# Performance work log

Measured on AMD Instinct MI355X. Metric: run time of the kernel, lower is better.

## Reference

```python
import jax, jax.numpy as jnp
import numpy as np

N = 4096
PED_SPEED = 1.34   # desired pedestrian speed (m/s)
K = 2.0            # goal-attraction gain
ALPHA = 10.66      # repulsion strength
PED_RADIUS = 0.3
PED_MASS = 60.0
BETTA = 0.71       # repulsion range
DT = 0.4
COST_A = 1.0       # goal-progress weight
COST_B = 1.0       # blame (proximity) weight
COST_E = 1.0       # blame length scale
EPS = 1e-8


def calc_forces(state, goals):
    pos = state[:, 0:2]            # [N,2]
    vel = state[:, 2:4]            # [N,2]
    # O(N^2) pairwise social repulsion
    delta = pos[:, None, :] - pos[None, :, :]                    # [N,N,2]
    dist = jnp.sqrt(jnp.sum(delta * delta, axis=-1) + EPS)       # [N,N]
    mag = ALPHA * jnp.exp((2.0 * PED_RADIUS - dist) / BETTA)     # [N,N]
    mag = mag * (1.0 - jnp.eye(pos.shape[0], dtype=pos.dtype))   # zero self-force
    rep_force = jnp.sum((mag / dist)[..., None] * delta, axis=1)  # [N,2]
    # attraction toward goal: relax velocity to desired velocity
    to_goal = goals - pos
    gd = jnp.sqrt(jnp.sum(to_goal * to_goal, axis=-1, keepdims=True) + EPS)
    attr_force = K * PED_MASS * (PED_SPEED * to_goal / gd - vel)
    return rep_force, attr_force


def pose_propagation(F, state):
    pos = state[:, 0:2]
    vel = state[:, 2:4]
    vel_new = vel + (F / PED_MASS) * DT
    speed = jnp.sqrt(jnp.sum(vel_new * vel_new, axis=-1, keepdims=True) + EPS)
    vel_new = vel_new * jnp.minimum(1.0, PED_SPEED / speed)  # clamp to max speed
    pos_new = pos + vel_new * DT
    return jnp.concatenate([pos_new, vel_new], axis=1)      # [N,4]


def calc_cost_function(goals, robot_init_pose, state, observed_state):
    pos = state[:, 0:2]
    robot_pose = pos[0]  # agent 0 is the robot
    goal_vec = goals[0] - robot_init_pose
    pg = jnp.dot(pos[0] - robot_init_pose, goal_vec) / (jnp.sqrt(jnp.sum(goal_vec * goal_vec)) + EPS)
    dist_rp = jnp.sqrt(jnp.sum((pos - robot_pose) ** 2, axis=-1) + EPS)  # [N]
    blame = COST_B * jnp.exp(-dist_rp / COST_E)
    dev = jnp.sum((pos - observed_state[:, 0:2]) ** 2, axis=-1)
    return -COST_A * pg + blame + dev  # [N]


def setup_inputs():
    key = jax.random.key(0)
    k1, k2, k3, k4 = jax.random.split(key, 4)
    scale = jnp.array([10.0, 10.0, 1.0, 1.0], dtype=jnp.float32)
    state = jax.random.normal(k1, (N, 4), dtype=jnp.float32) * scale
    goals = jax.random.normal(k2, (N, 2), dtype=jnp.float32) * 10.0
    robot_init_pose = jax.random.normal(k3, (2,), dtype=jnp.float32) * 10.0
    observed_state = jax.random.normal(k4, (N, 4), dtype=jnp.float32) * scale
    cost = jnp.zeros((N, 1), dtype=jnp.float32)
    return {"state": state, "cost": cost, "goals": goals,
            "robot_init_pose": robot_init_pose, "observed_state": observed_state}


def reference(state, cost, goals, robot_init_pose, observed_state):
    rf, af = calc_forces(state, goals)
    F = rf + af
    out = pose_propagation(F, state)
    temp = calc_cost_function(goals, robot_init_pose, out, observed_state)
    cost_new = cost + temp.reshape(-1, 1)
    return out, cost_new
```

## Files before the change

kernel.cpp:

```cpp
#include <hip/hip_runtime.h>

#define N 4096
#define NBJ 64
#define EPS 1e-8f

typedef float v2f __attribute__((ext_vector_type(2)));

__global__ __launch_bounds__(256) void rep_pairs(const float4* __restrict__ state4,
                                                 float2* __restrict__ part) {
    __shared__ float sx[64];
    __shared__ float sy[64];
    const int tid = threadIdx.x;
    const int jb  = blockIdx.y;
    const int i   = blockIdx.x * 256 + tid;

    if (tid < 64) {
        const float4 s = state4[jb * 64 + tid];
        sx[tid] = s.x;
        sy[tid] = s.y;
    }
    const float4 si = state4[i];
    __syncthreads();

    const float C1 = 1.44269504088896340736f / 0.71f;
    const float C0 = 0.6f * C1 + 3.41414351f;

    const v2f xi  = {si.x, si.x};
    const v2f yi  = {si.y, si.y};
    const v2f eps = {EPS, EPS};
    v2f fx0 = {0.f, 0.f}, fy0 = {0.f, 0.f};
    v2f fx1 = {0.f, 0.f}, fy1 = {0.f, 0.f};

#pragma unroll 8
    for (int jj = 0; jj < 64; jj += 4) {
        {
            const v2f X = *(const v2f*)&sx[jj];
            const v2f Y = *(const v2f*)&sy[jj];
            const v2f dx = xi - X;
            const v2f dy = yi - Y;
            const v2f r2 = dx * dx + (dy * dy + eps);
            v2f inv; inv.x = __builtin_amdgcn_rsqf(r2.x);
                     inv.y = __builtin_amdgcn_rsqf(r2.y);
            const v2f d   = r2 * inv;
            const v2f arg = C0 - C1 * d;
            v2f e; e.x = __builtin_amdgcn_exp2f(arg.x);
                   e.y = __builtin_amdgcn_exp2f(arg.y);
            const v2f coef = e * inv;
            fx0 += coef * dx;
            fy0 += coef * dy;
        }
        {
            const v2f X = *(const v2f*)&sx[jj + 2];
            const v2f Y = *(const v2f*)&sy[jj + 2];
            const v2f dx = xi - X;
            const v2f dy = yi - Y;
            const v2f r2 = dx * dx + (dy * dy + eps);
            v2f inv; inv.x = __builtin_amdgcn_rsqf(r2.x);
                     inv.y = __builtin_amdgcn_rsqf(r2.y);
            const v2f d   = r2 * inv;
            const v2f arg = C0 - C1 * d;
            v2f e; e.x = __builtin_amdgcn_exp2f(arg.x);
                   e.y = __builtin_amdgcn_exp2f(arg.y);
            const v2f coef = e * inv;
            fx1 += coef * dx;
            fy1 += coef * dy;
        }
    }
    const v2f fxs = fx0 + fx1, fys = fy0 + fy1;
    part[(size_t)jb * N + i] = make_float2(fxs.x + fxs.y, fys.x + fys.y);
}

__global__ __launch_bounds__(256) void finalize(const float4* __restrict__ state4,
                                                const float*  __restrict__ cost_in,
                                                const float*  __restrict__ goals,
                                                const float*  __restrict__ rip,
                                                const float4* __restrict__ obs4,
                                                const float2* __restrict__ part,
                                                float*        __restrict__ out) {
    __shared__ float4 red[4][64];
    __shared__ float2 s_p0;
    const int tid = threadIdx.x;
    const int ip  = tid & 63;
    const int ks  = tid >> 6;
    const int i0  = blockIdx.x * 128 + ip * 2;
    const float4* p4 = (const float4*)part;

    float4 acc = make_float4(0.f, 0.f, 0.f, 0.f);
    for (int k = ks * 16; k < ks * 16 + 16; ++k) {
        const float4 p = p4[(size_t)k * (N / 2) + (i0 >> 1)];
        acc.x += p.x; acc.y += p.y; acc.z += p.z; acc.w += p.w;
    }
    red[ks][ip] = acc;

    if (tid < 64) {
        float2 f0 = part[(size_t)tid * N];
#pragma unroll
        for (int off = 32; off > 0; off >>= 1) {
            f0.x += __shfl_down(f0.x, off);
            f0.y += __shfl_down(f0.y, off);
        }
        if (tid == 0) {
            const float4 s0 = state4[0];
            const float gx = goals[0] - s0.x, gy = goals[1] - s0.y;
            const float gd = sqrtf(fmaf(gx, gx, fmaf(gy, gy, EPS)));
            const float Fx0 = f0.x + 120.f * (1.34f * gx / gd - s0.z);
            const float Fy0 = f0.y + 120.f * (1.34f * gy / gd - s0.w);
            float vnx = fmaf(Fx0, 0.4f / 60.f, s0.z);
            float vny = fmaf(Fy0, 0.4f / 60.f, s0.w);
            const float sp  = sqrtf(fmaf(vnx, vnx, fmaf(vny, vny, EPS)));
            const float fac = fminf(1.f, 1.34f / sp);
            vnx *= fac; vny *= fac;
            s_p0 = make_float2(fmaf(vnx, 0.4f, s0.x), fmaf(vny, 0.4f, s0.y));
        }
    }
    __syncthreads();

    if (ks == 0) {
        float4 a = red[0][ip];
        const float4 b = red[1][ip], c = red[2][ip], d4 = red[3][ip];
        a.x += b.x + c.x + d4.x;
        a.y += b.y + c.y + d4.y;
        a.z += b.z + c.z + d4.z;
        a.w += b.w + c.w + d4.w;

        const float4 g2 = ((const float4*)goals)[i0 >> 1];
        const float2 ci = ((const float2*)cost_in)[i0 >> 1];
        const float rx = rip[0], ry = rip[1];
        const float gvx = goals[0] - rx, gvy = goals[1] - ry;
        const float inv_gl = 1.f / (sqrtf(gvx * gvx + gvy * gvy) + EPS);
        const float p0x = s_p0.x, p0y = s_p0.y;
        const float pg = ((p0x - rx) * gvx + (p0y - ry) * gvy) * inv_gl;

        float2 cost_out;
#pragma unroll
        for (int u = 0; u < 2; ++u) {
            const int ia = i0 + u;
            float Fx = u ? a.z : a.x;
            float Fy = u ? a.w : a.y;
            const float4 s = state4[ia];
            const float gx = (u ? g2.z : g2.x) - s.x;
            const float gy = (u ? g2.w : g2.y) - s.y;
            const float gd = sqrtf(fmaf(gx, gx, fmaf(gy, gy, EPS)));
            Fx += 120.f * (1.34f * gx / gd - s.z);
            Fy += 120.f * (1.34f * gy / gd - s.w);
            float vnx = fmaf(Fx, 0.4f / 60.f, s.z);
            float vny = fmaf(Fy, 0.4f / 60.f, s.w);
            const float sp  = sqrtf(fmaf(vnx, vnx, fmaf(vny, vny, EPS)));
            const float fac = fminf(1.f, 1.34f / sp);
            vnx *= fac; vny *= fac;
            const float pnx = fmaf(vnx, 0.4f, s.x);
            const float pny = fmaf(vny, 0.4f, s.y);

            ((float4*)out)[ia] = make_float4(pnx, pny, vnx, vny);

            const float ddx = pnx - p0x, ddy = pny - p0y;
            const float dist_rp = sqrtf(fmaf(ddx, ddx, fmaf(ddy, ddy, EPS)));
            const float blame = __expf(-dist_rp);
            const float4 ob = obs4[ia];
            const float dev = (pnx - ob.x) * (pnx - ob.x) + (pny - ob.y) * (pny - ob.y);
            const float cv = (u ? ci.y : ci.x) + (-pg + blame + dev);
            if (u) cost_out.y = cv; else cost_out.x = cv;
        }
        ((float2*)(out + 4 * N))[i0 >> 1] = cost_out;
    }
}

extern "C" void kernel_launch(void* const* d_in, const int* in_sizes, int n_in,
                              void* d_out, int out_size, void* d_ws, size_t ws_size,
                              hipStream_t stream) {
    const float* state = (const float*)d_in[0];
    const float* cost  = (const float*)d_in[1];
    const float* goals = (const float*)d_in[2];
    const float* rip   = (const float*)d_in[3];
    const float* obs   = (const float*)d_in[4];
    float* out   = (float*)d_out;
    float2* part = (float2*)d_ws;

    rep_pairs<<<dim3(16, NBJ), 256, 0, stream>>>((const float4*)state, part);
    finalize<<<N / 128, 256, 0, stream>>>((const float4*)state, cost, goals, rip,
                                          (const float4*)obs, part, out);
}
```

Measured before the change: 69.52 us.

## Fuse pairwise repulsion and finalize into one kernel with in-block reduction

After: 69.26 us. About the same (-0.4%).

```diff
diff --git a/kernel.cpp b/kernel.cpp
--- a/kernel.cpp
+++ b/kernel.cpp
@@ -1,167 +1,177 @@
 #include <hip/hip_runtime.h>
 
 #define N 4096
-#define NBJ 64
 #define EPS 1e-8f
+#define BLK 512
+#define APB 8
 
 typedef float v2f __attribute__((ext_vector_type(2)));
 
-__global__ __launch_bounds__(256) void rep_pairs(const float4* __restrict__ state4,
-                                                 float2* __restrict__ part) {
-    __shared__ float sx[64];
-    __shared__ float sy[64];
+__global__ __launch_bounds__(BLK) void fused(const float4* __restrict__ state4,
+                                             const float*  __restrict__ cost_in,
+                                             const float*  __restrict__ goals,
+                                             const float*  __restrict__ rip,
+                                             const float4* __restrict__ obs4,
+                                             float*        __restrict__ out) {
+    __shared__ float  sx[N];
+    __shared__ float  sy[N];
+    __shared__ float4 red[BLK / 64][4];
+    __shared__ float2 red0[BLK / 64];
+
     const int tid = threadIdx.x;
-    const int jb  = blockIdx.y;
-    const int i   = blockIdx.x * 256 + tid;
+    const int blk = blockIdx.x;
 
-    if (tid < 64) {
-        const float4 s = state4[jb * 64 + tid];
-        sx[tid] = s.x;
-        sy[tid] = s.y;
+#pragma unroll
+    for (int m = 0; m < 4; ++m) {
+        const int j0 = 2 * tid + 1024 * m;
+        const float4 a = state4[j0];
+        const float4 b = state4[j0 + 1];
+        *(v2f*)&sx[j0] = (v2f){a.x, b.x};
+        *(v2f*)&sy[j0] = (v2f){a.y, b.y};
     }
-    const float4 si = state4[i];
+
+    const int il = tid & 3;
+    const int ks = tid >> 2;
+    const int a0 = blk * APB + 2 * il;
+    const float4 sA = state4[a0];
+    const float4 sB = state4[a0 + 1];
     __syncthreads();
 
     const float C1 = 1.44269504088896340736f / 0.71f;
     const float C0 = 0.6f * C1 + 3.41414351f;
 
-    const v2f xi  = {si.x, si.x};
-    const v2f yi  = {si.y, si.y};
-    const v2f eps = {EPS, EPS};
-    v2f fx0 = {0.f, 0.f}, fy0 = {0.f, 0.f};
-    v2f fx1 = {0.f, 0.f}, fy1 = {0.f, 0.f};
+    const v2f eps2 = {EPS, EPS};
+    const v2f xA = {sA.x, sA.x}, yA = {sA.y, sA.y};
+    const v2f xB = {sB.x, sB.x}, yB = {sB.y, sB.y};
+    v2f fxA = {0.f, 0.f}, fyA = {0.f, 0.f};
+    v2f fxB = {0.f, 0.f}, fyB = {0.f, 0.f};
 
-#pragma unroll 8
-    for (int jj = 0; jj < 64; jj += 4) {
-        {
-            const v2f X = *(const v2f*)&sx[jj];
-            const v2f Y = *(const v2f*)&sy[jj];
-            const v2f dx = xi - X;
-            const v2f dy = yi - Y;
-            const v2f r2 = dx * dx + (dy * dy + eps);
-            v2f inv; inv.x = __builtin_amdgcn_rsqf(r2.x);
-                     inv.y = __builtin_amdgcn_rsqf(r2.y);
-            const v2f d   = r2 * inv;
-            const v2f arg = C0 - C1 * d;
-            v2f e; e.x = __builtin_amdgcn_exp2f(arg.x);
-                   e.y = __builtin_amdgcn_exp2f(arg.y);
-            const v2f coef = e * inv;
-            fx0 += coef * dx;
-            fy0 += coef * dy;
-        }
-        {
-            const v2f X = *(const v2f*)&sx[jj + 2];
-            const v2f Y = *(const v2f*)&sy[jj + 2];
-            const v2f dx = xi - X;
-            const v2f dy = yi - Y;
-            const v2f r2 = dx * dx + (dy * dy + eps);
-            v2f inv; inv.x = __builtin_amdgcn_rsqf(r2.x);
-                     inv.y = __builtin_amdgcn_rsqf(r2.y);
-            const v2f d   = r2 * inv;
-            const v2f arg = C0 - C1 * d;
-            v2f e; e.x = __builtin_amdgcn_exp2f(arg.x);
-                   e.y = __builtin_amdgcn_exp2f(arg.y);
-            const v2f coef = e * inv;
-            fx1 += coef * dx;
-            fy1 += coef * dy;
+#pragma unroll
+    for (int c = 0; c < 8; ++c) {
+        const int j0 = (ks << 5) + (((c + ks) & 7) << 2);
+        const float4 X = *(const float4*)&sx[j0];
+        const float4 Y = *(const float4*)&sy[j0];
+        const v2f Xp[2] = {{X.x, X.y}, {X.z, X.w}};
+        const v2f Yp[2] = {{Y.x, Y.y}, {Y.z, Y.w}};
+#pragma unroll
+        for (int h = 0; h < 2; ++h) {
+            {
+                const v2f dx = xA - Xp[h];
+                const v2f dy = yA - Yp[h];
+                const v2f r2 = dx * dx + (dy * dy + eps2);
+                v2f inv; inv.x = __builtin_amdgcn_rsqf(r2.x);
+                         inv.y = __builtin_amdgcn_rsqf(r2.y);
+                const v2f d   = r2 * inv;
+                const v2f arg = C0 - C1 * d;
+                v2f e; e.x = __builtin_amdgcn_exp2f(arg.x);
+                       e.y = __builtin_amdgcn_exp2f(arg.y);
+                const v2f coef = e * inv;
+                fxA += coef * dx;
+                fyA += coef * dy;
+            }
+            {
+                const v2f dx = xB - Xp[h];
+                const v2f dy = yB - Yp[h];
+                const v2f r2 = dx * dx + (dy * dy + eps2);
+                v2f inv; inv.x = __builtin_amdgcn_rsqf(r2.x);
+                         inv.y = __builtin_amdgcn_rsqf(r2.y);
+                const v2f d   = r2 * inv;
+                const v2f arg = C0 - C1 * d;
+                v2f e; e.x = __builtin_amdgcn_exp2f(arg.x);
+                       e.y = __builtin_amdgcn_exp2f(arg.y);
+                const v2f coef = e * inv;
+                fxB += coef * dx;
+                fyB += coef * dy;
+            }
         }
     }
-    const v2f fxs = fx0 + fx1, fys = fy0 + fy1;
-    part[(size_t)jb * N + i] = make_float2(fxs.x + fxs.y, fys.x + fys.y);
-}
 
-__global__ __launch_bounds__(256) void finalize(const float4* __restrict__ state4,
-                                                const float*  __restrict__ cost_in,
-                                                const float*  __restrict__ goals,
-                                                const float*  __restrict__ rip,
-                                                const float4* __restrict__ obs4,
-                                                const float2* __restrict__ part,
-                                                float*        __restrict__ out) {
-    __shared__ float4 red[4][64];
-    __shared__ float2 s_p0;
-    const int tid = threadIdx.x;
-    const int ip  = tid & 63;
-    const int ks  = tid >> 6;
-    const int i0  = blockIdx.x * 128 + ip * 2;
-    const float4* p4 = (const float4*)part;
-
-    float4 acc = make_float4(0.f, 0.f, 0.f, 0.f);
-    for (int k = ks * 16; k < ks * 16 + 16; ++k) {
-        const float4 p = p4[(size_t)k * (N / 2) + (i0 >> 1)];
-        acc.x += p.x; acc.y += p.y; acc.z += p.z; acc.w += p.w;
-    }
-    red[ks][ip] = acc;
-
-    if (tid < 64) {
-        float2 f0 = part[(size_t)tid * N];
+    float f0x = 0.f, f0y = 0.f;
+    {
+        const float x0 = sx[0], y0 = sy[0];
 #pragma unroll
-        for (int off = 32; off > 0; off >>= 1) {
-            f0.x += __shfl_down(f0.x, off);
-            f0.y += __shfl_down(f0.y, off);
-        }
-        if (tid == 0) {
-            const float4 s0 = state4[0];
-            const float gx = goals[0] - s0.x, gy = goals[1] - s0.y;
-            const float gd = sqrtf(fmaf(gx, gx, fmaf(gy, gy, EPS)));
-            const float Fx0 = f0.x + 120.f * (1.34f * gx / gd - s0.z);
-            const float Fy0 = f0.y + 120.f * (1.34f * gy / gd - s0.w);
-            float vnx = fmaf(Fx0, 0.4f / 60.f, s0.z);
-            float vny = fmaf(Fy0, 0.4f / 60.f, s0.w);
-            const float sp  = sqrtf(fmaf(vnx, vnx, fmaf(vny, vny, EPS)));
-            const float fac = fminf(1.f, 1.34f / sp);
-            vnx *= fac; vny *= fac;
-            s_p0 = make_float2(fmaf(vnx, 0.4f, s0.x), fmaf(vny, 0.4f, s0.y));
+        for (int m = 0; m < 8; ++m) {
+            const int j = tid + (m << 9);
+            const float dx = x0 - sx[j];
+            const float dy = y0 - sy[j];
+            const float r2 = fmaf(dx, dx, fmaf(dy, dy, EPS));
+            const float inv = __builtin_amdgcn_rsqf(r2);
+            const float d   = r2 * inv;
+            const float coef = __builtin_amdgcn_exp2f(fmaf(-C1, d, C0)) * inv;
+            f0x = fmaf(coef, dx, f0x);
+            f0y = fmaf(coef, dy, f0y);
         }
     }
+
+    float FxA = fxA.x + fxA.y, FyA = fyA.x + fyA.y;
+    float FxB = fxB.x + fxB.y, FyB = fyB.x + fyB.y;
+#pragma unroll
+    for (int off = 4; off <= 32; off <<= 1) {
+        FxA += __shfl_xor(FxA, off);
+        FyA += __shfl_xor(FyA, off);
+        FxB += __shfl_xor(FxB, off);
+        FyB += __shfl_xor(FyB, off);
+    }
+#pragma unroll
+    for (int off = 1; off <= 32; off <<= 1) {
+        f0x += __shfl_xor(f0x, off);
+        f0y += __shfl_xor(f0y, off);
+    }
+    const int wv = tid >> 6, ln = tid & 63;
+    if (ln < 4)  red[wv][ln] = make_float4(FxA, FyA, FxB, FyB);
+    if (ln == 0) red0[wv] = make_float2(f0x, f0y);
     __syncthreads();
 
-    if (ks == 0) {
-        float4 a = red[0][ip];
-        const float4 b = red[1][ip], c = red[2][ip], d4 = red[3][ip];
-        a.x += b.x + c.x + d4.x;
-        a.y += b.y + c.y + d4.y;
-        a.z += b.z + c.z + d4.z;
-        a.w += b.w + c.w + d4.w;
+    if (tid < APB) {
+        float Fx = 0.f, Fy = 0.f, F0x = 0.f, F0y = 0.f;
+#pragma unroll
+        for (int w = 0; w < BLK / 64; ++w) {
+            const float4 r = red[w][tid >> 1];
+            Fx += (tid & 1) ? r.z : r.x;
+            Fy += (tid & 1) ? r.w : r.y;
+            const float2 r0 = red0[w];
+            F0x += r0.x; F0y += r0.y;
+        }
 
-        const float4 g2 = ((const float4*)goals)[i0 >> 1];
-        const float2 ci = ((const float2*)cost_in)[i0 >> 1];
+        const float4 s0 = state4[0];
+        const float g0x = goals[0] - s0.x, g0y = goals[1] - s0.y;
+        const float gd0 = sqrtf(fmaf(g0x, g0x, fmaf(g0y, g0y, EPS)));
+        F0x += 120.f * (1.34f * g0x / gd0 - s0.z);
+        F0y += 120.f * (1.34f * g0y / gd0 - s0.w);
+        float v0x = fmaf(F0x, 0.4f / 60.f, s0.z);
+        float v0y = fmaf(F0y, 0.4f / 60.f, s0.w);
+        const float sp0 = sqrtf(fmaf(v0x, v0x, fmaf(v0y, v0y, EPS)));
+        const float fc0 = fminf(1.f, 1.34f / sp0);
+        v0x *= fc0; v0y *= fc0;
+        const float p0x = fmaf(v0x, 0.4f, s0.x);
+        const float p0y = fmaf(v0y, 0.4f, s0.y);
+
+        const int ia = blk * APB + tid;
+        const float4 s = state4[ia];
+        const float gx = goals[2 * ia]     - s.x;
+        const float gy = goals[2 * ia + 1] - s.y;
+        const float gd = sqrtf(fmaf(gx, gx, fmaf(gy, gy, EPS)));
+        Fx += 120.f * (1.34f * gx / gd - s.z);
+        Fy += 120.f * (1.34f * gy / gd - s.w);
+        float vnx = fmaf(Fx, 0.4f / 60.f, s.z);
+        float vny = fmaf(Fy, 0.4f / 60.f, s.w);
+        const float sp = sqrtf(fmaf(vnx, vnx, fmaf(vny, vny, EPS)));
+        const float fc = fminf(1.f, 1.34f / sp);
+        vnx *= fc; vny *= fc;
+        const float pnx = fmaf(vnx, 0.4f, s.x);
+        const float pny = fmaf(vny, 0.4f, s.y);
+        ((float4*)out)[ia] = make_float4(pnx, pny, vnx, vny);
+
         const float rx = rip[0], ry = rip[1];
         const float gvx = goals[0] - rx, gvy = goals[1] - ry;
         const float inv_gl = 1.f / (sqrtf(gvx * gvx + gvy * gvy) + EPS);
-        const float p0x = s_p0.x, p0y = s_p0.y;
         const float pg = ((p0x - rx) * gvx + (p0y - ry) * gvy) * inv_gl;
-
-        float2 cost_out;
-#pragma unroll
-        for (int u = 0; u < 2; ++u) {
-            const int ia = i0 + u;
-            float Fx = u ? a.z : a.x;
-            float Fy = u ? a.w : a.y;
-            const float4 s = state4[ia];
-            const float gx = (u ? g2.z : g2.x) - s.x;
-            const float gy = (u ? g2.w : g2.y) - s.y;
-            const float gd = sqrtf(fmaf(gx, gx, fmaf(gy, gy, EPS)));
-            Fx += 120.f * (1.34f * gx / gd - s.z);
-            Fy += 120.f * (1.34f * gy / gd - s.w);
-            float vnx = fmaf(Fx, 0.4f / 60.f, s.z);
-            float vny = fmaf(Fy, 0.4f / 60.f, s.w);
-            const float sp  = sqrtf(fmaf(vnx, vnx, fmaf(vny, vny, EPS)));
-            const float fac = fminf(1.f, 1.34f / sp);
-            vnx *= fac; vny *= fac;
-            const float pnx = fmaf(vnx, 0.4f, s.x);
-            const float pny = fmaf(vny, 0.4f, s.y);
-
-            ((float4*)out)[ia] = make_float4(pnx, pny, vnx, vny);
-
-            const float ddx = pnx - p0x, ddy = pny - p0y;
-            const float dist_rp = sqrtf(fmaf(ddx, ddx, fmaf(ddy, ddy, EPS)));
-            const float blame = __expf(-dist_rp);
-            const float4 ob = obs4[ia];
-            const float dev = (pnx - ob.x) * (pnx - ob.x) + (pny - ob.y) * (pny - ob.y);
-            const float cv = (u ? ci.y : ci.x) + (-pg + blame + dev);
-            if (u) cost_out.y = cv; else cost_out.x = cv;
-        }
-        ((float2*)(out + 4 * N))[i0 >> 1] = cost_out;
+        const float ddx = pnx - p0x, ddy = pny - p0y;
+        const float dist_rp = sqrtf(fmaf(ddx, ddx, fmaf(ddy, ddy, EPS)));
+        const float blame = __expf(-dist_rp);
+        const float4 ob = obs4[ia];
+        const float dev = (pnx - ob.x) * (pnx - ob.x) + (pny - ob.y) * (pny - ob.y);
+        out[4 * N + ia] = cost_in[ia] + (-pg + blame + dev);
     }
 }
 
@@ -173,10 +183,9 @@
     const float* goals = (const float*)d_in[2];
     const float* rip   = (const float*)d_in[3];
     const float* obs   = (const float*)d_in[4];
-    float* out   = (float*)d_out;
-    float2* part = (float2*)d_ws;
+    float* out = (float*)d_out;
+    (void)d_ws; (void)ws_size;
 
-    rep_pairs<<<dim3(16, NBJ), 256, 0, stream>>>((const float4*)state, part);
-    finalize<<<N / 128, 256, 0, stream>>>((const float4*)state, cost, goals, rip,
-                                          (const float4*)obs, part, out);
+    fused<<<N / APB, BLK, 0, stream>>>((const float4*)state, cost, goals, rip,
+                                       (const float4*)obs, out);
 }
```
